# Kernel tuning notes

Measured on AMD Instinct MI355X. Metric: run time of the kernel, lower is better.

Reference implementation:

```python
import jax, jax.numpy as jnp
import numpy as np

NEG_INF = -10000.0
ALPHA = 0.2      # LeakyReLU slope
EPS = 1e-5       # LayerNorm eps
B, N, D = 8, 2048, 128


def setup_inputs() -> dict:
    key = jax.random.key(0)
    ks = jax.random.split(key, 8)
    x = jax.random.normal(ks[0], (B, N, D), dtype=jnp.float32)
    adj_bool = jax.random.randint(ks[1], (B, N, N), 0, 2, dtype=jnp.int32)
    node_mask = jax.random.randint(ks[2], (B, N), 0, 2, dtype=jnp.int32)
    s = 1.0 / np.sqrt(D)
    W = jax.random.uniform(ks[3], (D, D), jnp.float32, -s, s)    # fc weight (in->out)
    a_l = jax.random.uniform(ks[4], (D,), jnp.float32, -s, s)    # attn_l weight
    a_r = jax.random.uniform(ks[5], (D,), jnp.float32, -s, s)    # attn_r weight
    gamma = jnp.ones((D,), jnp.float32)                          # LayerNorm weight
    beta = jnp.zeros((D,), jnp.float32)                          # LayerNorm bias
    return {"x": x, "adj_bool": adj_bool, "node_mask": node_mask,
            "W": W, "a_l": a_l, "a_r": a_r, "gamma": gamma, "beta": beta}


def reference(x, adj_bool, node_mask, W, a_l, a_r, gamma, beta):
    m = node_mask.astype(x.dtype)[..., None]           # [B,N,1]
    x = x * m
    h = jnp.einsum('bnd,de->bne', x, W)                # [B,N,D]
    e_l = jnp.einsum('bnd,d->bn', h, a_l)              # [B,N]
    e_r = jnp.einsum('bnd,d->bn', h, a_r)              # [B,N]
    e = e_l[:, :, None] + e_r[:, None, :]              # [B,N,N]
    e = jnp.where(e > 0, e, ALPHA * e)                 # LeakyReLU
    pair = (node_mask[:, :, None] * node_mask[:, None, :]) > 0
    allowed = (adj_bool > 0) & pair
    e = jnp.where(allowed, e, NEG_INF)
    attn = jax.nn.softmax(e, axis=-1)                  # finite (NEG_INF fill), nan_to_num is a no-op
    out = jnp.einsum('bij,bjd->bid', attn, h)          # dropout in eval mode = identity
    out = (out + x) * m                                # residual (ind==outd), then node mask
    mu = jnp.mean(out, axis=-1, keepdims=True)
    var = jnp.var(out, axis=-1, keepdims=True)
    out = (out - mu) * jax.lax.rsqrt(var + EPS) * gamma + beta
    return out
```

## Files before the change

kernel.cpp:

```cpp
#include <hip/hip_runtime.h>
#include <stdint.h>


#define BB 8
#define NN 2048
#define DD 128
#define GAT_NEG_INF -10000.0f
#define LN_EPS 1e-5f

typedef __attribute__((ext_vector_type(8))) short short8;
typedef __attribute__((ext_vector_type(4))) float f32x4;

__device__ __forceinline__ unsigned pk_bf16(float a, float b) {
    unsigned ua = __float_as_uint(a); ua += 0x7FFFu + ((ua >> 16) & 1u);
    unsigned ub = __float_as_uint(b); ub += 0x7FFFu + ((ub >> 16) & 1u);
    return (ua >> 16) | (ub & 0xFFFF0000u);
}

__global__ __launch_bounds__(256) void fc_kernel(
    const float* __restrict__ x, const int* __restrict__ mask,
    const float* __restrict__ W, const float* __restrict__ a_l,
    const float* __restrict__ a_r, unsigned short* __restrict__ hT,
    float* __restrict__ el, float* __restrict__ er)
{
    __shared__ __align__(16) float Ws[64 * DD];
    __shared__ __align__(16) float xs[32 * 68];

    const int t  = threadIdx.x;
    const int b  = blockIdx.x >> 6;
    const int it = blockIdx.x & 63;
    const int i0 = it * 32;

    const int r  = t >> 3;
    const int c  = t & 7;
    const int o0 = c * 16;

    float acc[16];
#pragma unroll
    for (int u = 0; u < 16; ++u) acc[u] = 0.f;

    for (int kt = 0; kt < 2; ++kt) {
        __syncthreads();
        const float4* W4  = (const float4*)(W + (size_t)kt * 64 * DD);
        float4*       Ws4 = (float4*)Ws;
#pragma unroll
        for (int i = 0; i < 8; ++i) Ws4[t + 256 * i] = W4[t + 256 * i];
#pragma unroll
        for (int i = 0; i < 2; ++i) {
            int idx = t + 256 * i;
            int row = idx >> 4, c4 = idx & 15;
            float4 v = *(const float4*)(x + ((size_t)(b * NN + i0 + row)) * DD
                                          + kt * 64 + c4 * 4);
            float mm = (float)mask[b * NN + i0 + row];
            v.x *= mm; v.y *= mm; v.z *= mm; v.w *= mm;
            *(float4*)(xs + row * 68 + c4 * 4) = v;
        }
        __syncthreads();

        const float4* Wsr = (const float4*)Ws;
#pragma unroll 4
        for (int k = 0; k < 64; ++k) {
            float xv = xs[r * 68 + k];
#pragma unroll
            for (int u4 = 0; u4 < 4; ++u4) {
                float4 w = Wsr[k * 32 + c * 4 + u4];
                acc[u4 * 4 + 0] += xv * w.x;
                acc[u4 * 4 + 1] += xv * w.y;
                acc[u4 * 4 + 2] += xv * w.z;
                acc[u4 * 4 + 3] += xv * w.w;
            }
        }
    }

    float sl = 0.f, sr = 0.f;
#pragma unroll
    for (int u = 0; u < 16; ++u) {
        sl += acc[u] * a_l[o0 + u];
        sr += acc[u] * a_r[o0 + u];
    }
#pragma unroll
    for (int off = 4; off; off >>= 1) {
        sl += __shfl_xor(sl, off, 8);
        sr += __shfl_xor(sr, off, 8);
    }
    if (c == 0) {
        el[b * NN + i0 + r] = sl;
        er[b * NN + i0 + r] = sr;
    }

    __syncthreads();
    float* hTs = Ws;
#pragma unroll
    for (int u = 0; u < 16; ++u) hTs[(o0 + u) * 33 + r] = acc[u];
    __syncthreads();

    {
        int d = t >> 1, half = t & 1;
        const float* src = hTs + d * 33 + half * 16;
        unsigned pk8[8];
#pragma unroll
        for (int k = 0; k < 8; ++k) pk8[k] = pk_bf16(src[2 * k], src[2 * k + 1]);
        unsigned short* dst = hT + ((size_t)(b * DD + d)) * NN + i0 + half * 16;
        *(uint4*)dst       = make_uint4(pk8[0], pk8[1], pk8[2], pk8[3]);
        *(uint4*)(dst + 8) = make_uint4(pk8[4], pk8[5], pk8[6], pk8[7]);
    }
}

__global__ __launch_bounds__(64) void attn_kernel(
    const float* __restrict__ x, const int* __restrict__ adj,
    const int* __restrict__ mask, const unsigned short* __restrict__ hT,
    const float* __restrict__ el, const float* __restrict__ er,
    const float* __restrict__ gamma, const float* __restrict__ beta,
    float* __restrict__ outp)
{
    const int lane = threadIdx.x;
    const int row  = lane & 15;
    const int grp  = lane >> 4;
    const int b    = blockIdx.x >> 7;
    const int it   = blockIdx.x & 127;
    const int i0   = it * 16;
    const int gi   = i0 + row;

    const float el_r = el[b * NN + gi];
    const int   mi   = mask[b * NN + gi];
    const int*  adj_row = adj + ((size_t)(b * NN + gi)) * NN;
    const float* er_b = er + b * NN;
    const int*   mk_b = mask + b * NN;
    const unsigned short* hT_b = hT + (size_t)b * DD * NN;

    f32x4 acc[8];
#pragma unroll
    for (int nb = 0; nb < 8; ++nb) acc[nb] = (f32x4)0.f;
    float m_run = -3.0e38f, l_run = 0.f;

    int4 pa0, pa1, pa2, pa3;
    float4 pe0, pe1, pe2, pe3;
    int4 pq0, pq1, pq2, pq3;

    auto load_meta = [&](int jt) {
        const int jb = jt * 64 + grp * 8;
        pa0 = *(const int4*)(adj_row + jb);
        pa1 = *(const int4*)(adj_row + jb + 4);
        pa2 = *(const int4*)(adj_row + jb + 32);
        pa3 = *(const int4*)(adj_row + jb + 36);
        pe0 = *(const float4*)(er_b + jb);
        pe1 = *(const float4*)(er_b + jb + 4);
        pe2 = *(const float4*)(er_b + jb + 32);
        pe3 = *(const float4*)(er_b + jb + 36);
        pq0 = *(const int4*)(mk_b + jb);
        pq1 = *(const int4*)(mk_b + jb + 4);
        pq2 = *(const int4*)(mk_b + jb + 32);
        pq3 = *(const int4*)(mk_b + jb + 36);
    };
    load_meta(0);

    union BU { int4 q; short8 v; };
    union AU { unsigned u[4]; short8 v; };

#pragma unroll 1
    for (int jt = 0; jt < NN / 64; ++jt) {
        int4 a0 = pa0, a1 = pa1, a2 = pa2, a3 = pa3;
        float4 e0 = pe0, e1 = pe1, e2 = pe2, e3 = pe3;
        int4 q0 = pq0, q1 = pq1, q2 = pq2, q3 = pq3;
        load_meta(jt < NN / 64 - 1 ? jt + 1 : jt);

        BU bf[16];
        {
            const int jb = jt * 64 + grp * 8;
#pragma unroll
            for (int s = 0; s < 2; ++s)
#pragma unroll
                for (int nb = 0; nb < 8; ++nb)
                    bf[s * 8 + nb].q = *(const int4*)(hT_b
                        + (size_t)(nb * 16 + row) * NN + jb + s * 32);
        }

        int   av[16] = {a0.x,a0.y,a0.z,a0.w, a1.x,a1.y,a1.z,a1.w,
                        a2.x,a2.y,a2.z,a2.w, a3.x,a3.y,a3.z,a3.w};
        int   qv[16] = {q0.x,q0.y,q0.z,q0.w, q1.x,q1.y,q1.z,q1.w,
                        q2.x,q2.y,q2.z,q2.w, q3.x,q3.y,q3.z,q3.w};
        float ev[16] = {e0.x,e0.y,e0.z,e0.w, e1.x,e1.y,e1.z,e1.w,
                        e2.x,e2.y,e2.z,e2.w, e3.x,e3.y,e3.z,e3.w};
        float ss[16];
        float tmax = -3.0e38f;
#pragma unroll
        for (int u = 0; u < 16; ++u) {
            float e = el_r + ev[u];
            e = fmaxf(e, 0.2f * e);
            bool ok = (av[u] & qv[u] & mi) != 0;
            ss[u] = ok ? e : GAT_NEG_INF;
            tmax = fmaxf(tmax, ss[u]);
        }
        tmax = fmaxf(tmax, __shfl_xor(tmax, 16, 64));
        tmax = fmaxf(tmax, __shfl_xor(tmax, 32, 64));
        float m_new = fmaxf(m_run, tmax);
        float al    = __expf(m_run - m_new);
        float p[16];
        float psum = 0.f;
#pragma unroll
        for (int u = 0; u < 16; ++u) {
            p[u] = __expf(ss[u] - m_new);
            psum += p[u];
        }
        psum += __shfl_xor(psum, 16, 64);
        psum += __shfl_xor(psum, 32, 64);
        l_run = l_run * al + psum;
        m_run = m_new;

        float alr[4];
#pragma unroll
        for (int reg = 0; reg < 4; ++reg) alr[reg] = __shfl(al, grp * 4 + reg, 64);
#pragma unroll
        for (int nb = 0; nb < 8; ++nb) {
            acc[nb][0] *= alr[0]; acc[nb][1] *= alr[1];
            acc[nb][2] *= alr[2]; acc[nb][3] *= alr[3];
        }

        AU A0, A1;
#pragma unroll
        for (int k = 0; k < 4; ++k) {
            A0.u[k] = pk_bf16(p[2 * k],     p[2 * k + 1]);
            A1.u[k] = pk_bf16(p[8 + 2 * k], p[8 + 2 * k + 1]);
        }

#pragma unroll
        for (int nb = 0; nb < 8; ++nb)
            acc[nb] = __builtin_amdgcn_mfma_f32_16x16x32_bf16(A0.v, bf[nb].v, acc[nb], 0, 0, 0);
#pragma unroll
        for (int nb = 0; nb < 8; ++nb)
            acc[nb] = __builtin_amdgcn_mfma_f32_16x16x32_bf16(A1.v, bf[8 + nb].v, acc[nb], 0, 0, 0);
    }

    float inv[4], mq[4];
#pragma unroll
    for (int reg = 0; reg < 4; ++reg) {
        float lq = __shfl(l_run, grp * 4 + reg, 64);
        inv[reg] = 1.0f / lq;
        mq[reg]  = (float)mk_b[i0 + grp * 4 + reg];
    }

    float v[8][4];
    float s1[4] = {0.f, 0.f, 0.f, 0.f}, s2[4] = {0.f, 0.f, 0.f, 0.f};
#pragma unroll
    for (int nb = 0; nb < 8; ++nb)
#pragma unroll
        for (int reg = 0; reg < 4; ++reg) {
            float xv = x[((size_t)(b * NN + i0 + grp * 4 + reg)) * DD + nb * 16 + row];
            float tv = (acc[nb][reg] * inv[reg] + xv) * mq[reg];
            v[nb][reg] = tv;
            s1[reg] += tv;
            s2[reg] += tv * tv;
        }
#pragma unroll
    for (int off = 1; off < 16; off <<= 1)
#pragma unroll
        for (int reg = 0; reg < 4; ++reg) {
            s1[reg] += __shfl_xor(s1[reg], off, 64);
            s2[reg] += __shfl_xor(s2[reg], off, 64);
        }

    float mu[4], rsd[4];
#pragma unroll
    for (int reg = 0; reg < 4; ++reg) {
        mu[reg] = s1[reg] * (1.0f / DD);
        float var = s2[reg] * (1.0f / DD) - mu[reg] * mu[reg];
        rsd[reg] = rsqrtf(var + LN_EPS);
    }
#pragma unroll
    for (int nb = 0; nb < 8; ++nb) {
        float g  = gamma[nb * 16 + row];
        float be = beta[nb * 16 + row];
#pragma unroll
        for (int reg = 0; reg < 4; ++reg) {
            float o = (v[nb][reg] - mu[reg]) * rsd[reg] * g + be;
            outp[((size_t)(b * NN + i0 + grp * 4 + reg)) * DD + nb * 16 + row] = o;
        }
    }
}

extern "C" void kernel_launch(void* const* d_in, const int* in_sizes, int n_in,
                              void* d_out, int out_size, void* d_ws, size_t ws_size,
                              hipStream_t stream) {
    const float* x     = (const float*)d_in[0];
    const int*   adj   = (const int*)d_in[1];
    const int*   maskp = (const int*)d_in[2];
    const float* W     = (const float*)d_in[3];
    const float* a_l   = (const float*)d_in[4];
    const float* a_r   = (const float*)d_in[5];
    const float* gamma = (const float*)d_in[6];
    const float* beta  = (const float*)d_in[7];
    float*       outp  = (float*)d_out;

    unsigned short* hT = (unsigned short*)d_ws;
    float* el = (float*)(hT + (size_t)BB * DD * NN);
    float* er = el + (size_t)BB * NN;

    fc_kernel<<<BB * (NN / 32), 256, 0, stream>>>(x, maskp, W, a_l, a_r, hT, el, er);
    attn_kernel<<<BB * (NN / 16), 64, 0, stream>>>(x, adj, maskp, hT, el, er,
                                                   gamma, beta, outp);
}
```

Measured before the change: 278.3 us.

## Split attention key range across four waves with LDS flash-softmax merge

Each attention block now runs four wavefronts instead of one. Every wave processes a quarter of the key tiles for the same 16 query rows, keeping its own running max and sum. The partial accumulators, maxes and sums go to shared memory, are merged with rescaling, and the LayerNorm epilogue is recomputed with row-per-16-thread float4 loads and stores. The aim is more in-flight memory traffic and shorter serial loops per wave, at the cost of an LDS reduction, a block barrier and extra shared-memory use per block.

Measured after the change: 275.5 us. No clear change (-1.0%).

```diff
diff --git a/kernel.cpp b/kernel.cpp
--- a/kernel.cpp
+++ b/kernel.cpp
@@ -106,14 +106,20 @@
     }
 }
 
-__global__ __launch_bounds__(64) void attn_kernel(
+__global__ __launch_bounds__(256, 4) void attn_kernel(
     const float* __restrict__ x, const int* __restrict__ adj,
     const int* __restrict__ mask, const unsigned short* __restrict__ hT,
     const float* __restrict__ el, const float* __restrict__ er,
     const float* __restrict__ gamma, const float* __restrict__ beta,
     float* __restrict__ outp)
 {
-    const int lane = threadIdx.x;
+    __shared__ __align__(16) float sAcc[4][16][132];
+    __shared__ float sM[4][16];
+    __shared__ float sL[4][16];
+
+    const int t    = threadIdx.x;
+    const int w    = t >> 6;
+    const int lane = t & 63;
     const int row  = lane & 15;
     const int grp  = lane >> 4;
     const int b    = blockIdx.x >> 7;
@@ -132,6 +138,9 @@
 #pragma unroll
     for (int nb = 0; nb < 8; ++nb) acc[nb] = (f32x4)0.f;
     float m_run = -3.0e38f, l_run = 0.f;
+
+    const int jt_begin = w * (NN / 64 / 4);
+    const int jt_end   = jt_begin + (NN / 64 / 4);
 
     int4 pa0, pa1, pa2, pa3;
     float4 pe0, pe1, pe2, pe3;
@@ -152,17 +161,17 @@
         pq2 = *(const int4*)(mk_b + jb + 32);
         pq3 = *(const int4*)(mk_b + jb + 36);
     };
-    load_meta(0);
+    load_meta(jt_begin);
 
     union BU { int4 q; short8 v; };
     union AU { unsigned u[4]; short8 v; };
 
 #pragma unroll 1
-    for (int jt = 0; jt < NN / 64; ++jt) {
+    for (int jt = jt_begin; jt < jt_end; ++jt) {
         int4 a0 = pa0, a1 = pa1, a2 = pa2, a3 = pa3;
         float4 e0 = pe0, e1 = pe1, e2 = pe2, e3 = pe3;
         int4 q0 = pq0, q1 = pq1, q2 = pq2, q3 = pq3;
-        load_meta(jt < NN / 64 - 1 ? jt + 1 : jt);
+        load_meta(jt < jt_end - 1 ? jt + 1 : jt);
 
         BU bf[16];
         {
@@ -231,50 +240,69 @@
             acc[nb] = __builtin_amdgcn_mfma_f32_16x16x32_bf16(A1.v, bf[8 + nb].v, acc[nb], 0, 0, 0);
     }
 
-    float inv[4], mq[4];
-#pragma unroll
-    for (int reg = 0; reg < 4; ++reg) {
-        float lq = __shfl(l_run, grp * 4 + reg, 64);
-        inv[reg] = 1.0f / lq;
-        mq[reg]  = (float)mk_b[i0 + grp * 4 + reg];
-    }
-
-    float v[8][4];
-    float s1[4] = {0.f, 0.f, 0.f, 0.f}, s2[4] = {0.f, 0.f, 0.f, 0.f};
 #pragma unroll
     for (int nb = 0; nb < 8; ++nb)
 #pragma unroll
-        for (int reg = 0; reg < 4; ++reg) {
-            float xv = x[((size_t)(b * NN + i0 + grp * 4 + reg)) * DD + nb * 16 + row];
-            float tv = (acc[nb][reg] * inv[reg] + xv) * mq[reg];
-            v[nb][reg] = tv;
-            s1[reg] += tv;
-            s2[reg] += tv * tv;
-        }
-#pragma unroll
-    for (int off = 1; off < 16; off <<= 1)
-#pragma unroll
-        for (int reg = 0; reg < 4; ++reg) {
-            s1[reg] += __shfl_xor(s1[reg], off, 64);
-            s2[reg] += __shfl_xor(s2[reg], off, 64);
-        }
-
-    float mu[4], rsd[4];
-#pragma unroll
-    for (int reg = 0; reg < 4; ++reg) {
-        mu[reg] = s1[reg] * (1.0f / DD);
-        float var = s2[reg] * (1.0f / DD) - mu[reg] * mu[reg];
-        rsd[reg] = rsqrtf(var + LN_EPS);
-    }
-#pragma unroll
-    for (int nb = 0; nb < 8; ++nb) {
-        float g  = gamma[nb * 16 + row];
-        float be = beta[nb * 16 + row];
-#pragma unroll
-        for (int reg = 0; reg < 4; ++reg) {
-            float o = (v[nb][reg] - mu[reg]) * rsd[reg] * g + be;
-            outp[((size_t)(b * NN + i0 + grp * 4 + reg)) * DD + nb * 16 + row] = o;
-        }
+        for (int reg = 0; reg < 4; ++reg)
+            sAcc[w][grp * 4 + reg][nb * 16 + row] = acc[nb][reg];
+    if (grp == 0) { sM[w][row] = m_run; sL[w][row] = l_run; }
+    __syncthreads();
+
+    const int crow = t >> 4;
+    const int cl   = t & 15;
+    const int gr   = i0 + crow;
+
+    float mw0 = sM[0][crow], mw1 = sM[1][crow], mw2 = sM[2][crow], mw3 = sM[3][crow];
+    float M = fmaxf(fmaxf(mw0, mw1), fmaxf(mw2, mw3));
+    float sc0 = __expf(mw0 - M), sc1 = __expf(mw1 - M);
+    float sc2 = __expf(mw2 - M), sc3 = __expf(mw3 - M);
+    float Lsum = sL[0][crow] * sc0 + sL[1][crow] * sc1
+               + sL[2][crow] * sc2 + sL[3][crow] * sc3;
+    const float linv = 1.0f / Lsum;
+    const float mrow = (float)mk_b[gr];
+    const float* xrow = x + ((size_t)(b * NN + gr)) * DD;
+
+    float vbuf[8];
+    float s1 = 0.f, s2 = 0.f;
+#pragma unroll
+    for (int h = 0; h < 2; ++h) {
+        const int c0 = cl * 8 + h * 4;
+        float4 xv = *(const float4*)(xrow + c0);
+        float4 a0 = *(const float4*)(&sAcc[0][crow][c0]);
+        float4 a1 = *(const float4*)(&sAcc[1][crow][c0]);
+        float4 a2 = *(const float4*)(&sAcc[2][crow][c0]);
+        float4 a3 = *(const float4*)(&sAcc[3][crow][c0]);
+        float tv;
+        tv = ((a0.x*sc0 + a1.x*sc1 + a2.x*sc2 + a3.x*sc3) * linv + xv.x) * mrow;
+        vbuf[h*4+0] = tv; s1 += tv; s2 += tv*tv;
+        tv = ((a0.y*sc0 + a1.y*sc1 + a2.y*sc2 + a3.y*sc3) * linv + xv.y) * mrow;
+        vbuf[h*4+1] = tv; s1 += tv; s2 += tv*tv;
+        tv = ((a0.z*sc0 + a1.z*sc1 + a2.z*sc2 + a3.z*sc3) * linv + xv.z) * mrow;
+        vbuf[h*4+2] = tv; s1 += tv; s2 += tv*tv;
+        tv = ((a0.w*sc0 + a1.w*sc1 + a2.w*sc2 + a3.w*sc3) * linv + xv.w) * mrow;
+        vbuf[h*4+3] = tv; s1 += tv; s2 += tv*tv;
+    }
+#pragma unroll
+    for (int off = 1; off < 16; off <<= 1) {
+        s1 += __shfl_xor(s1, off, 64);
+        s2 += __shfl_xor(s2, off, 64);
+    }
+    const float mu  = s1 * (1.0f / DD);
+    const float var = s2 * (1.0f / DD) - mu * mu;
+    const float rsd = rsqrtf(var + LN_EPS);
+
+    float* orow = outp + ((size_t)(b * NN + gr)) * DD;
+#pragma unroll
+    for (int h = 0; h < 2; ++h) {
+        const int c0 = cl * 8 + h * 4;
+        float4 g  = *(const float4*)(gamma + c0);
+        float4 be = *(const float4*)(beta + c0);
+        float4 o;
+        o.x = (vbuf[h*4+0] - mu) * rsd * g.x + be.x;
+        o.y = (vbuf[h*4+1] - mu) * rsd * g.y + be.y;
+        o.z = (vbuf[h*4+2] - mu) * rsd * g.z + be.z;
+        o.w = (vbuf[h*4+3] - mu) * rsd * g.w + be.w;
+        *(float4*)(orow + c0) = o;
     }
 }
 
@@ -296,6 +324,6 @@
     float* er = el + (size_t)BB * NN;
 
     fc_kernel<<<BB * (NN / 32), 256, 0, stream>>>(x, maskp, W, a_l, a_r, hT, el, er);
-    attn_kernel<<<BB * (NN / 16), 64, 0, stream>>>(x, adj, maskp, hT, el, er,
-                                                   gamma, beta, outp);
+    attn_kernel<<<BB * (NN / 16), 256, 0, stream>>>(x, adj, maskp, hT, el, er,
+                                                    gamma, beta, outp);
 }
```
